# Performance work log

Measured on AMD Instinct MI355X. Metric: run time of the kernel, lower is better.

## Reference

```python
import jax, jax.numpy as jnp
import numpy as np

B, N, C = 4, 4096, 256
H, D, K = 8, 32, 16  # heads, dim_head, knn


def setup_inputs() -> dict:
    key = jax.random.key(0)
    ks = jax.random.split(key, 7)
    s = 1.0 / np.sqrt(C)
    return {
        "x": jax.random.normal(ks[0], (B, N, C), dtype=jnp.float32),
        "Wq": jax.random.normal(ks[1], (C, H * D), dtype=jnp.float32) * s,
        "bq": jnp.zeros((H * D,), dtype=jnp.float32),
        "Wk": jax.random.normal(ks[2], (C, H * D), dtype=jnp.float32) * s,
        "bk": jnp.zeros((H * D,), dtype=jnp.float32),
        "Wv": jax.random.normal(ks[3], (C, H * D), dtype=jnp.float32) * s,
        "bv": jnp.zeros((H * D,), dtype=jnp.float32),
    }


def _knn_indices(x):
    # squared euclidean distances per batch: [B, N, N]
    sq = jnp.sum(x * x, axis=-1)
    d2 = sq[:, :, None] + sq[:, None, :] - 2.0 * jnp.einsum("bnc,bmc->bnm", x, x)
    # exclude self-loops (loop=False)
    eye = jnp.eye(x.shape[1], dtype=bool)
    d2 = jnp.where(eye[None], jnp.inf, d2)
    # k nearest neighbors (smallest distance)
    _, idx = jax.lax.top_k(-d2, K)  # [B, N, K]
    return idx


def reference(x, Wq, bq, Wk, bk, Wv, bv):
    idx = _knn_indices(x)  # [B, N, K] neighbor (source) node ids per target node
    # gather neighbor features: [B, N, K, C]
    xj = jax.vmap(lambda xb, ib: xb[ib])(x, idx)
    q = (x @ Wq + bq).reshape(B, N, H, D)           # target-node queries
    ke = (xj @ Wk + bk).reshape(B, N, K, H, D)      # per-edge keys
    ve = (xj @ Wv + bv).reshape(B, N, K, H, D)      # per-edge values
    scale = 1.0 / np.sqrt(D)
    scores = jnp.einsum("bnhd,bnkhd->bnkh", q, ke) * scale
    alpha = jax.nn.softmax(scores, axis=2)          # softmax over each node's K neighbors
    out = jnp.einsum("bnkh,bnkhd->bnhd", alpha, ve)
    return out.reshape(B, N, H * D)
```

## Files before the change

kernel.cpp:

```cpp
#include <hip/hip_runtime.h>
#include <cstdint>
#include <cstddef>

#define N_ 4096
#define C_ 256

typedef _Float16 h8 __attribute__((ext_vector_type(8)));
typedef _Float16 h4 __attribute__((ext_vector_type(4)));
typedef float f4 __attribute__((ext_vector_type(4)));

__device__ __forceinline__ void gl2lds16(const void* g, void* l) {
  __builtin_amdgcn_global_load_lds((const __attribute__((address_space(1))) void*)g,
                                   (__attribute__((address_space(3))) void*)l, 16, 0, 0);
}

__device__ __forceinline__ void ce_asc(double& a, double& b) {
  double mn = fmin(a, b), mx = fmax(a, b);
  a = mn; b = mx;
}

__device__ __forceinline__ void sort8_asc(double* c) {
#pragma unroll
  for (int k = 2; k <= 8; k <<= 1)
#pragma unroll
    for (int j = k >> 1; j > 0; j >>= 1)
#pragma unroll
      for (int i = 0; i < 8; i++) {
        int l = i ^ j;
        if (l > i) {
          bool up = ((i & k) == 0);
          double a = c[i], b = c[l];
          double mn = fmin(a, b), mx = fmax(a, b);
          c[i] = up ? mn : mx;
          c[l] = up ? mx : mn;
        }
      }
}

__device__ __forceinline__ void merge8_top16(double* karr, const double* c) {
#pragma unroll
  for (int i = 0; i < 8; i++)
    karr[8 + i] = fmin(karr[8 + i], c[7 - i]);
#pragma unroll
  for (int j = 8; j > 0; j >>= 1)
#pragma unroll
    for (int i = 0; i < 16; i++) {
      int l = i ^ j;
      if (l > i) ce_asc(karr[i], karr[l]);
    }
}

__device__ __forceinline__ void merge16d(double* a, const double* b) {
#pragma unroll
  for (int i = 0; i < 16; i++) a[i] = fmin(a[i], b[15 - i]);
#pragma unroll
  for (int j = 8; j > 0; j >>= 1)
#pragma unroll
    for (int i = 0; i < 16; i++) {
      int l = i ^ j;
      if (l > i) {
        double mn = fmin(a[i], a[l]), mx = fmax(a[i], a[l]);
        a[i] = mn; a[l] = mx;
      }
    }
}

__global__ __launch_bounds__(256) void k_prep(const float* __restrict__ x,
                                              float* __restrict__ sq,
                                              _Float16* __restrict__ xh,
                                              _Float16* __restrict__ xl) {
  int wave = threadIdx.x >> 6, lane = threadIdx.x & 63;
  int row = blockIdx.x * 4 + wave;
  size_t off = (size_t)row * C_ + lane * 4;
  float4 v = *(const float4*)(x + off);
  h4 hi; hi[0] = (_Float16)v.x; hi[1] = (_Float16)v.y;
         hi[2] = (_Float16)v.z; hi[3] = (_Float16)v.w;
  h4 lo; lo[0] = (_Float16)(v.x - (float)hi[0]); lo[1] = (_Float16)(v.y - (float)hi[1]);
         lo[2] = (_Float16)(v.z - (float)hi[2]); lo[3] = (_Float16)(v.w - (float)hi[3]);
  *(h4*)(xh + off) = hi;
  *(h4*)(xl + off) = lo;
  float s = v.x * v.x + v.y * v.y + v.z * v.z + v.w * v.w;
  s += __shfl_xor(s, 32); s += __shfl_xor(s, 16); s += __shfl_xor(s, 8);
  s += __shfl_xor(s, 4);  s += __shfl_xor(s, 2);  s += __shfl_xor(s, 1);
  if (lane == 0) sq[row] = s;
}

__global__ __launch_bounds__(256) void k_wsplit(const float* __restrict__ Wq,
                                                const float* __restrict__ Wk,
                                                const float* __restrict__ Wv,
                                                _Float16* __restrict__ wh,
                                                _Float16* __restrict__ wl) {
  int g = blockIdx.x * 256 + threadIdx.x;
  int m = g >> 16, e = g & 65535;
  int k = e >> 8, j = e & 255;
  const float* W = (m == 0) ? Wq : ((m == 1) ? Wk : Wv);
  float v = W[k * 256 + j];
  _Float16 hi = (_Float16)v;
  _Float16 lo = (_Float16)(v - (float)hi);
  wh[m * 65536 + j * 256 + k] = hi;
  wl[m * 65536 + j * 256 + k] = lo;
}

__global__ __launch_bounds__(256, 3) void k_proj(const _Float16* __restrict__ xh,
                                                 const _Float16* __restrict__ xl,
                                                 const _Float16* __restrict__ wh,
                                                 const _Float16* __restrict__ wl,
                                                 const float* __restrict__ bqp,
                                                 const float* __restrict__ bkp,
                                                 const float* __restrict__ bvp,
                                                 float* __restrict__ qf,
                                                 float* __restrict__ kf,
                                                 float* __restrict__ vf) {
  int tid = threadIdx.x;
  int bid = blockIdx.x;
  int m   = bid >> 8;
  int rb  = (bid >> 1) & 127;
  int cp  = bid & 1;
  int wave = tid >> 6, lane = tid & 63, quad = lane >> 4, l16 = lane & 15;
  const float* bb = (m == 0) ? bqp : ((m == 1) ? bkp : bvp);
  float* dst      = (m == 0) ? qf  : ((m == 1) ? kf  : vf);
  int row0 = rb * 128 + wave * 32;

  h8 Ah[2][8], Al[2][8];
#pragma unroll
  for (int rt = 0; rt < 2; rt++)
#pragma unroll
    for (int kc = 0; kc < 8; kc++) {
      size_t off = (size_t)(row0 + rt * 16 + l16) * C_ + kc * 32 + quad * 8;
      Ah[rt][kc] = *(const h8*)(xh + off);
      Al[rt][kc] = *(const h8*)(xl + off);
    }
  const _Float16* whm = wh + (size_t)m * 65536;
  const _Float16* wlm = wl + (size_t)m * 65536;

  f4 acc[2][8];
#pragma unroll
  for (int rt = 0; rt < 2; rt++)
#pragma unroll
    for (int ct = 0; ct < 8; ct++) acc[rt][ct] = f4{0.f, 0.f, 0.f, 0.f};
#pragma unroll
  for (int kc = 0; kc < 8; kc++) {
#pragma unroll
    for (int ct = 0; ct < 8; ct++) {
      int col = cp * 128 + ct * 16 + l16;
      h8 bh = *(const h8*)(whm + (size_t)col * 256 + kc * 32 + quad * 8);
      h8 bl = *(const h8*)(wlm + (size_t)col * 256 + kc * 32 + quad * 8);
#pragma unroll
      for (int rt = 0; rt < 2; rt++) {
        acc[rt][ct] = __builtin_amdgcn_mfma_f32_16x16x32_f16(Ah[rt][kc], bh, acc[rt][ct], 0, 0, 0);
        acc[rt][ct] = __builtin_amdgcn_mfma_f32_16x16x32_f16(Ah[rt][kc], bl, acc[rt][ct], 0, 0, 0);
        acc[rt][ct] = __builtin_amdgcn_mfma_f32_16x16x32_f16(Al[rt][kc], bh, acc[rt][ct], 0, 0, 0);
      }
    }
  }
#pragma unroll
  for (int rt = 0; rt < 2; rt++)
#pragma unroll
    for (int ct = 0; ct < 8; ct++) {
      int col = cp * 128 + ct * 16 + l16;
      float bias = bb[col];
#pragma unroll
      for (int i = 0; i < 4; i++) {
        int r = row0 + rt * 16 + quad * 4 + i;
        dst[(size_t)r * C_ + col] = acc[rt][ct][i] + bias;
      }
    }
}

__global__ __launch_bounds__(256, 2) void k_knn(const _Float16* __restrict__ xh,
                                                const _Float16* __restrict__ xl,
                                                const float* __restrict__ sq,
                                                double* __restrict__ pd) {
  __shared__ __align__(16) _Float16 Bh[2][16 * 528];
  __shared__ __align__(16) _Float16 Bl[2][16 * 528];
  __shared__ __align__(16) float sc[4][16 * 36];

  int tid = threadIdx.x;
  int wave = tid >> 6, lane = tid & 63, quad = lane >> 4, l16 = lane & 15;
  int bid = blockIdx.x;
  int s4 = bid & 3, tile = (bid >> 2) & 31, b = bid >> 7;
  int bN = b * N_, n0 = tile * 128, src0g = s4 * 1024;

  h8 Ah[2][8], Al[2][8];
  int tb = bN + n0 + wave * 32;
#pragma unroll
  for (int rt = 0; rt < 2; rt++)
#pragma unroll
    for (int kc = 0; kc < 8; kc++) {
      size_t off = (size_t)(tb + rt * 16 + l16) * C_ + kc * 32 + quad * 8;
      Ah[rt][kc] = *(const h8*)(xh + off);
      Al[rt][kc] = *(const h8*)(xl + off);
    }
  float sqT[2][4];
#pragma unroll
  for (int rt = 0; rt < 2; rt++)
#pragma unroll
    for (int i = 0; i < 4; i++)
      sqT[rt][i] = sq[tb + rt * 16 + quad * 4 + i];

  double karr[16];
#pragma unroll
  for (int p = 0; p < 16; p++) karr[p] = 1e300;
  int rloc = lane & 31;
  int half = lane >> 5;
  int rown = wave * 32 + rloc;
  int rt_owner = rloc >> 4;
  int rl = rloc & 15;

  {
    const _Float16* gh = xh + (size_t)(bN + src0g) * C_ + lane * 8;
    const _Float16* gl = xl + (size_t)(bN + src0g) * C_ + lane * 8;
#pragma unroll
    for (int k = 0; k < 4; k++) {
      int seg = wave * 4 + k;
      gl2lds16(gh + seg * 512, &Bh[0][seg * 528]);
      gl2lds16(gl + seg * 512, &Bl[0][seg * 528]);
    }
  }

  int hb0 = ((l16 >> 1) * 528) + ((l16 & 1) * 256) + quad * 8;
  int hb1 = (((16 + l16) >> 1) * 528) + ((l16 & 1) * 256) + quad * 8;

#pragma unroll 1
  for (int ch = 0; ch < 32; ch++) {
    int src0 = src0g + ch * 32;
    int buf = ch & 1;
    __syncthreads();

    if (ch < 31) {
      int srcn = src0 + 32;
      const _Float16* gh = xh + (size_t)(bN + srcn) * C_ + lane * 8;
      const _Float16* gl = xl + (size_t)(bN + srcn) * C_ + lane * 8;
#pragma unroll
      for (int k = 0; k < 4; k++) {
        int seg = wave * 4 + k;
        gl2lds16(gh + seg * 512, &Bh[buf ^ 1][seg * 528]);
        gl2lds16(gl + seg * 512, &Bl[buf ^ 1][seg * 528]);
      }
    }
    float sqc0 = sq[bN + src0 + l16];
    float sqc1 = sq[bN + src0 + 16 + l16];

    f4 acc[2][2];
#pragma unroll
    for (int rt = 0; rt < 2; rt++)
#pragma unroll
      for (int ct = 0; ct < 2; ct++) acc[rt][ct] = f4{0.f, 0.f, 0.f, 0.f};
#pragma unroll
    for (int kc = 0; kc < 8; kc++) {
      h8 bh0 = *(const h8*)(&Bh[buf][hb0 + kc * 32]);
      h8 bh1 = *(const h8*)(&Bh[buf][hb1 + kc * 32]);
      h8 bl0 = *(const h8*)(&Bl[buf][hb0 + kc * 32]);
      h8 bl1 = *(const h8*)(&Bl[buf][hb1 + kc * 32]);
#pragma unroll
      for (int rt = 0; rt < 2; rt++) {
        acc[rt][0] = __builtin_amdgcn_mfma_f32_16x16x32_f16(Ah[rt][kc], bh0, acc[rt][0], 0, 0, 0);
        acc[rt][0] = __builtin_amdgcn_mfma_f32_16x16x32_f16(Ah[rt][kc], bl0, acc[rt][0], 0, 0, 0);
        acc[rt][0] = __builtin_amdgcn_mfma_f32_16x16x32_f16(Al[rt][kc], bh0, acc[rt][0], 0, 0, 0);
        acc[rt][1] = __builtin_amdgcn_mfma_f32_16x16x32_f16(Ah[rt][kc], bh1, acc[rt][1], 0, 0, 0);
        acc[rt][1] = __builtin_amdgcn_mfma_f32_16x16x32_f16(Ah[rt][kc], bl1, acc[rt][1], 0, 0, 0);
        acc[rt][1] = __builtin_amdgcn_mfma_f32_16x16x32_f16(Al[rt][kc], bh1, acc[rt][1], 0, 0, 0);
      }
    }

    float dv[16];
#pragma unroll
    for (int rt = 0; rt < 2; rt++) {
#pragma unroll
      for (int ct = 0; ct < 2; ct++) {
        int c = ct * 16 + l16;
        float sqSr = ct ? sqc1 : sqc0;
#pragma unroll
        for (int i = 0; i < 4; i++) {
          int r = wave * 32 + rt * 16 + quad * 4 + i;
          float d2 = sqT[rt][i] + sqSr - 2.0f * acc[rt][ct][i];
          if (n0 + r == src0 + c) d2 = 1e38f;
          sc[wave][(quad * 4 + i) * 36 + c] = d2;
        }
      }
      if (rt_owner == rt) {
#pragma unroll
        for (int j = 0; j < 4; j++)
          *(float4*)&dv[j * 4] = *(const float4*)(&sc[wave][rl * 36 + half * 16 + j * 4]);
      }
      asm volatile("" ::: "memory");
    }

#pragma unroll
    for (int bt = 0; bt < 2; bt++) {
      double c8[8];
#pragma unroll
      for (int j = 0; j < 8; j++) {
        double key = (double)dv[bt * 8 + j];
        c8[j] = __longlong_as_double(__double_as_longlong(key) |
                                     (unsigned)(src0 + half * 16 + bt * 8 + j));
      }
      sort8_asc(c8);
      merge8_top16(karr, c8);
    }
  }

  __syncthreads();
  double* scd = (double*)&Bh[0][0];
  if (half) {
#pragma unroll
    for (int p = 0; p < 16; p++) scd[rown * 17 + p] = karr[p];
  }
  __syncthreads();
  if (!half) {
#pragma unroll
    for (int i = 0; i < 16; i++)
      karr[i] = fmin(karr[i], scd[rown * 17 + (15 - i)]);
#pragma unroll
    for (int j = 8; j > 0; j >>= 1)
#pragma unroll
      for (int i = 0; i < 16; i++) {
        int l = i ^ j;
        if (l > i) ce_asc(karr[i], karr[l]);
      }
#pragma unroll
    for (int p = 0; p < 16; p++)
      pd[((size_t)bid * 128 + rown) * 16 + p] = karr[p];
  }
}

__global__ __launch_bounds__(64) void k_kmerge(const double* __restrict__ pd,
                                               int* __restrict__ idxo) {
  int g = blockIdx.x * 64 + threadIdx.x;
  int b = g >> 12, n = g & 4095;
  int tile = n >> 7, r = n & 127;
  size_t base = (size_t)(((b * 32 + tile) * 4) * 128 + r) * 16;

  double acc[16], other[16];
#pragma unroll
  for (int p = 0; p < 16; p++) acc[p] = pd[base + p];
#pragma unroll
  for (int s = 1; s < 4; s++) {
    size_t bs = base + (size_t)s * 128 * 16;
#pragma unroll
    for (int p = 0; p < 16; p++) other[p] = pd[bs + p];
    merge16d(acc, other);
  }
#pragma unroll
  for (int k = 0; k < 16; k++)
    idxo[(size_t)g * 16 + k] = (int)(__double_as_longlong(acc[k]) & 0xFFF);
}

__global__ __launch_bounds__(256) void k_attn(const float* __restrict__ qf,
                                              const float* __restrict__ kf,
                                              const float* __restrict__ vf,
                                              const int* __restrict__ idxv,
                                              float* __restrict__ out) {
  int wave = threadIdx.x >> 6, lane = threadIdx.x & 63;
  int g = blockIdx.x * 4 + wave;
  int bN = (g >> 12) << 12;
  float4 q4 = *(const float4*)(qf + (size_t)g * C_ + lane * 4);
  int my = idxv[(size_t)g * 16 + (lane & 15)];
  const float scale = 0.17677669529663687f;

  float s[16];
  float4 vv[16];
#pragma unroll
  for (int j = 0; j < 16; j++) {
    int nb = __shfl(my, j);
    size_t base = (size_t)(bN + nb) * C_ + lane * 4;
    float4 k4 = *(const float4*)(kf + base);
    vv[j] = *(const float4*)(vf + base);
    float p = k4.x * q4.x + k4.y * q4.y + k4.z * q4.z + k4.w * q4.w;
    p += __shfl_xor(p, 1); p += __shfl_xor(p, 2); p += __shfl_xor(p, 4);
    s[j] = p * scale;
  }
  float mx = s[0];
#pragma unroll
  for (int j = 1; j < 16; j++) mx = fmaxf(mx, s[j]);
  float den = 0.f;
#pragma unroll
  for (int j = 0; j < 16; j++) { s[j] = __expf(s[j] - mx); den += s[j]; }
  float inv = 1.0f / den;
  float4 o; o.x = 0.f; o.y = 0.f; o.z = 0.f; o.w = 0.f;
#pragma unroll
  for (int j = 0; j < 16; j++) {
    float w = s[j] * inv;
    o.x = fmaf(w, vv[j].x, o.x); o.y = fmaf(w, vv[j].y, o.y);
    o.z = fmaf(w, vv[j].z, o.z); o.w = fmaf(w, vv[j].w, o.w);
  }
  *(float4*)(out + (size_t)g * C_ + lane * 4) = o;
}

extern "C" void kernel_launch(void* const* d_in, const int* in_sizes, int n_in,
                              void* d_out, int out_size, void* d_ws, size_t ws_size,
                              hipStream_t stream) {
  const float* x  = (const float*)d_in[0];
  const float* Wq = (const float*)d_in[1];
  const float* bq = (const float*)d_in[2];
  const float* Wk = (const float*)d_in[3];
  const float* bk = (const float*)d_in[4];
  const float* Wv = (const float*)d_in[5];
  const float* bv = (const float*)d_in[6];
  float* out = (float*)d_out;

  char* ws = (char*)d_ws;
  float*     sqp  = (float*)(ws + 0);
  _Float16*  xh   = (_Float16*)(ws + 65536);
  _Float16*  xl   = (_Float16*)(ws + 8454144);
  float*     qf   = (float*)(ws + 16842752);
  float*     kf   = (float*)(ws + 33619968);
  float*     vf   = (float*)(ws + 50397184);
  double*    pd   = (double*)(ws + 67174400);
  int*       idxb = (int*)  (ws + 75563008);
  _Float16*  whf  = (_Float16*)(ws + 76611584);
  _Float16*  wlf  = (_Float16*)(ws + 77004800);

  k_prep  <<<4096, 256, 0, stream>>>(x, sqp, xh, xl);
  k_wsplit<<<768,  256, 0, stream>>>(Wq, Wk, Wv, whf, wlf);
  k_proj  <<<768,  256, 0, stream>>>(xh, xl, whf, wlf, bq, bk, bv, qf, kf, vf);
  k_knn   <<<512,  256, 0, stream>>>(xh, xl, sqp, pd);
  k_kmerge<<<256,  64,  0, stream>>>(pd, idxb);
  k_attn  <<<4096, 256, 0, stream>>>(qf, kf, vf, idxb, out);
}
```

Measured before the change: 291.8 us.

## Transpose kNN MFMA so each lane owns a target, dropping LDS score shuffle

Reorganizes k_knn into 8 waves of 16 targets each. The MFMA operands are swapped so each lane's accumulator holds distances for its own target column. This removes the per-chunk LDS scratch round-trip that previously moved scores to the thread owning each row, and source squared norms now arrive through LDS via async global-to-LDS loads. Each lane sorts 8 candidates per chunk instead of 16, and the per-target top-16 lists held by four lanes are combined with a two-step LDS merge tree. The cost is more threads per block, extra barriers at the end, and higher register pressure under launch_bounds(512,4).

```diff
diff --git a/kernel.cpp b/kernel.cpp
--- a/kernel.cpp
+++ b/kernel.cpp
@@ -12,6 +12,10 @@
 __device__ __forceinline__ void gl2lds16(const void* g, void* l) {
   __builtin_amdgcn_global_load_lds((const __attribute__((address_space(1))) void*)g,
                                    (__attribute__((address_space(3))) void*)l, 16, 0, 0);
+}
+__device__ __forceinline__ void gl2lds4(const void* g, void* l) {
+  __builtin_amdgcn_global_load_lds((const __attribute__((address_space(1))) void*)g,
+                                   (__attribute__((address_space(3))) void*)l, 4, 0, 0);
 }
 
 __device__ __forceinline__ void ce_asc(double& a, double& b) {
@@ -167,13 +171,13 @@
     }
 }
 
-__global__ __launch_bounds__(256, 2) void k_knn(const _Float16* __restrict__ xh,
+__global__ __launch_bounds__(512, 4) void k_knn(const _Float16* __restrict__ xh,
                                                 const _Float16* __restrict__ xl,
                                                 const float* __restrict__ sq,
                                                 double* __restrict__ pd) {
   __shared__ __align__(16) _Float16 Bh[2][16 * 528];
   __shared__ __align__(16) _Float16 Bl[2][16 * 528];
-  __shared__ __align__(16) float sc[4][16 * 36];
+  __shared__ __align__(16) float sqLds[2][64];
 
   int tid = threadIdx.x;
   int wave = tid >> 6, lane = tid & 63, quad = lane >> 4, l16 = lane & 15;
@@ -181,45 +185,35 @@
   int s4 = bid & 3, tile = (bid >> 2) & 31, b = bid >> 7;
   int bN = b * N_, n0 = tile * 128, src0g = s4 * 1024;
 
-  h8 Ah[2][8], Al[2][8];
-  int tb = bN + n0 + wave * 32;
-#pragma unroll
-  for (int rt = 0; rt < 2; rt++)
-#pragma unroll
-    for (int kc = 0; kc < 8; kc++) {
-      size_t off = (size_t)(tb + rt * 16 + l16) * C_ + kc * 32 + quad * 8;
-      Ah[rt][kc] = *(const h8*)(xh + off);
-      Al[rt][kc] = *(const h8*)(xl + off);
-    }
-  float sqT[2][4];
-#pragma unroll
-  for (int rt = 0; rt < 2; rt++)
-#pragma unroll
-    for (int i = 0; i < 4; i++)
-      sqT[rt][i] = sq[tb + rt * 16 + quad * 4 + i];
+  h8 Th[8], Tl[8];
+  int tgt_loc = n0 + wave * 16 + l16;
+  int tgtg = bN + tgt_loc;
+#pragma unroll
+  for (int kc = 0; kc < 8; kc++) {
+    size_t off = (size_t)tgtg * C_ + kc * 32 + quad * 8;
+    Th[kc] = *(const h8*)(xh + off);
+    Tl[kc] = *(const h8*)(xl + off);
+  }
+  float sqT = sq[tgtg];
 
   double karr[16];
 #pragma unroll
   for (int p = 0; p < 16; p++) karr[p] = 1e300;
-  int rloc = lane & 31;
-  int half = lane >> 5;
-  int rown = wave * 32 + rloc;
-  int rt_owner = rloc >> 4;
-  int rl = rloc & 15;
 
   {
     const _Float16* gh = xh + (size_t)(bN + src0g) * C_ + lane * 8;
     const _Float16* gl = xl + (size_t)(bN + src0g) * C_ + lane * 8;
 #pragma unroll
-    for (int k = 0; k < 4; k++) {
-      int seg = wave * 4 + k;
+    for (int k = 0; k < 2; k++) {
+      int seg = wave * 2 + k;
       gl2lds16(gh + seg * 512, &Bh[0][seg * 528]);
       gl2lds16(gl + seg * 512, &Bl[0][seg * 528]);
     }
-  }
-
-  int hb0 = ((l16 >> 1) * 528) + ((l16 & 1) * 256) + quad * 8;
-  int hb1 = (((16 + l16) >> 1) * 528) + ((l16 & 1) * 256) + quad * 8;
+    if (wave == 0) gl2lds4(sq + bN + src0g + (lane & 31), &sqLds[0][0]);
+  }
+
+  int base0 = (l16 >> 1) * 528 + (l16 & 1) * 256 + quad * 8;
+  int base1 = base0 + 8 * 528;
 
 #pragma unroll 1
   for (int ch = 0; ch < 32; ch++) {
@@ -232,95 +226,79 @@
       const _Float16* gh = xh + (size_t)(bN + srcn) * C_ + lane * 8;
       const _Float16* gl = xl + (size_t)(bN + srcn) * C_ + lane * 8;
 #pragma unroll
-      for (int k = 0; k < 4; k++) {
-        int seg = wave * 4 + k;
+      for (int k = 0; k < 2; k++) {
+        int seg = wave * 2 + k;
         gl2lds16(gh + seg * 512, &Bh[buf ^ 1][seg * 528]);
         gl2lds16(gl + seg * 512, &Bl[buf ^ 1][seg * 528]);
       }
-    }
-    float sqc0 = sq[bN + src0 + l16];
-    float sqc1 = sq[bN + src0 + 16 + l16];
-
-    f4 acc[2][2];
-#pragma unroll
-    for (int rt = 0; rt < 2; rt++)
-#pragma unroll
-      for (int ct = 0; ct < 2; ct++) acc[rt][ct] = f4{0.f, 0.f, 0.f, 0.f};
+      if (wave == 0) gl2lds4(sq + bN + srcn + (lane & 31), &sqLds[buf ^ 1][0]);
+    }
+
+    f4 acc[2];
+    acc[0] = f4{0.f, 0.f, 0.f, 0.f};
+    acc[1] = f4{0.f, 0.f, 0.f, 0.f};
 #pragma unroll
     for (int kc = 0; kc < 8; kc++) {
-      h8 bh0 = *(const h8*)(&Bh[buf][hb0 + kc * 32]);
-      h8 bh1 = *(const h8*)(&Bh[buf][hb1 + kc * 32]);
-      h8 bl0 = *(const h8*)(&Bl[buf][hb0 + kc * 32]);
-      h8 bl1 = *(const h8*)(&Bl[buf][hb1 + kc * 32]);
-#pragma unroll
-      for (int rt = 0; rt < 2; rt++) {
-        acc[rt][0] = __builtin_amdgcn_mfma_f32_16x16x32_f16(Ah[rt][kc], bh0, acc[rt][0], 0, 0, 0);
-        acc[rt][0] = __builtin_amdgcn_mfma_f32_16x16x32_f16(Ah[rt][kc], bl0, acc[rt][0], 0, 0, 0);
-        acc[rt][0] = __builtin_amdgcn_mfma_f32_16x16x32_f16(Al[rt][kc], bh0, acc[rt][0], 0, 0, 0);
-        acc[rt][1] = __builtin_amdgcn_mfma_f32_16x16x32_f16(Ah[rt][kc], bh1, acc[rt][1], 0, 0, 0);
-        acc[rt][1] = __builtin_amdgcn_mfma_f32_16x16x32_f16(Ah[rt][kc], bl1, acc[rt][1], 0, 0, 0);
-        acc[rt][1] = __builtin_amdgcn_mfma_f32_16x16x32_f16(Al[rt][kc], bh1, acc[rt][1], 0, 0, 0);
-      }
-    }
-
-    float dv[16];
-#pragma unroll
-    for (int rt = 0; rt < 2; rt++) {
-#pragma unroll
-      for (int ct = 0; ct < 2; ct++) {
-        int c = ct * 16 + l16;
-        float sqSr = ct ? sqc1 : sqc0;
-#pragma unroll
-        for (int i = 0; i < 4; i++) {
-          int r = wave * 32 + rt * 16 + quad * 4 + i;
-          float d2 = sqT[rt][i] + sqSr - 2.0f * acc[rt][ct][i];
-          if (n0 + r == src0 + c) d2 = 1e38f;
-          sc[wave][(quad * 4 + i) * 36 + c] = d2;
-        }
-      }
-      if (rt_owner == rt) {
-#pragma unroll
-        for (int j = 0; j < 4; j++)
-          *(float4*)&dv[j * 4] = *(const float4*)(&sc[wave][rl * 36 + half * 16 + j * 4]);
-      }
-      asm volatile("" ::: "memory");
-    }
-
-#pragma unroll
-    for (int bt = 0; bt < 2; bt++) {
-      double c8[8];
-#pragma unroll
-      for (int j = 0; j < 8; j++) {
-        double key = (double)dv[bt * 8 + j];
-        c8[j] = __longlong_as_double(__double_as_longlong(key) |
-                                     (unsigned)(src0 + half * 16 + bt * 8 + j));
-      }
-      sort8_asc(c8);
-      merge8_top16(karr, c8);
-    }
+      h8 sh0 = *(const h8*)(&Bh[buf][base0 + kc * 32]);
+      h8 sh1 = *(const h8*)(&Bh[buf][base1 + kc * 32]);
+      h8 sl0 = *(const h8*)(&Bl[buf][base0 + kc * 32]);
+      h8 sl1 = *(const h8*)(&Bl[buf][base1 + kc * 32]);
+      acc[0] = __builtin_amdgcn_mfma_f32_16x16x32_f16(sh0, Th[kc], acc[0], 0, 0, 0);
+      acc[1] = __builtin_amdgcn_mfma_f32_16x16x32_f16(sh1, Th[kc], acc[1], 0, 0, 0);
+      acc[0] = __builtin_amdgcn_mfma_f32_16x16x32_f16(sh0, Tl[kc], acc[0], 0, 0, 0);
+      acc[1] = __builtin_amdgcn_mfma_f32_16x16x32_f16(sh1, Tl[kc], acc[1], 0, 0, 0);
+      acc[0] = __builtin_amdgcn_mfma_f32_16x16x32_f16(sl0, Th[kc], acc[0], 0, 0, 0);
+      acc[1] = __builtin_amdgcn_mfma_f32_16x16x32_f16(sl1, Th[kc], acc[1], 0, 0, 0);
+    }
+
+    const float* sqB = (const float*)&sqLds[buf][0];
+    double c8[8];
+#pragma unroll
+    for (int st = 0; st < 2; st++)
+#pragma unroll
+      for (int i = 0; i < 4; i++) {
+        int sidx = st * 16 + quad * 4 + i;
+        float d2 = sqT + sqB[sidx] - 2.0f * acc[st][i];
+        if (tgt_loc == src0 + sidx) d2 = 1e38f;
+        double key = (double)d2;
+        c8[st * 4 + i] = __longlong_as_double(__double_as_longlong(key) |
+                                              (unsigned)(src0 + sidx));
+      }
+    sort8_asc(c8);
+    merge8_top16(karr, c8);
   }
 
   __syncthreads();
-  double* scd = (double*)&Bh[0][0];
-  if (half) {
-#pragma unroll
-    for (int p = 0; p < 16; p++) scd[rown * 17 + p] = karr[p];
+  double* ex = (double*)&Bh[0][0];
+  if (quad >= 2) {
+    int slot = wave * 32 + (quad - 2) * 16 + l16;
+#pragma unroll
+    for (int p = 0; p < 16; p++) ex[slot * 16 + p] = karr[p];
   }
   __syncthreads();
-  if (!half) {
-#pragma unroll
-    for (int i = 0; i < 16; i++)
-      karr[i] = fmin(karr[i], scd[rown * 17 + (15 - i)]);
-#pragma unroll
-    for (int j = 8; j > 0; j >>= 1)
-#pragma unroll
-      for (int i = 0; i < 16; i++) {
-        int l = i ^ j;
-        if (l > i) ce_asc(karr[i], karr[l]);
-      }
+  if (quad < 2) {
+    double other[16];
+    int slot = wave * 32 + quad * 16 + l16;
+#pragma unroll
+    for (int p = 0; p < 16; p++) other[p] = ex[slot * 16 + p];
+    merge16d(karr, other);
+  }
+  __syncthreads();
+  if (quad == 1) {
+    int slot = wave * 16 + l16;
+#pragma unroll
+    for (int p = 0; p < 16; p++) ex[slot * 16 + p] = karr[p];
+  }
+  __syncthreads();
+  if (quad == 0) {
+    double other[16];
+    int slot = wave * 16 + l16;
+#pragma unroll
+    for (int p = 0; p < 16; p++) other[p] = ex[slot * 16 + p];
+    merge16d(karr, other);
 #pragma unroll
     for (int p = 0; p < 16; p++)
-      pd[((size_t)bid * 128 + rown) * 16 + p] = karr[p];
+      pd[((size_t)bid * 128 + wave * 16 + l16) * 16 + p] = karr[p];
   }
 }
 
@@ -414,7 +392,7 @@
   k_prep  <<<4096, 256, 0, stream>>>(x, sqp, xh, xl);
   k_wsplit<<<768,  256, 0, stream>>>(Wq, Wk, Wv, whf, wlf);
   k_proj  <<<768,  256, 0, stream>>>(xh, xl, whf, wlf, bq, bk, bv, qf, kf, vf);
-  k_knn   <<<512,  256, 0, stream>>>(xh, xl, sqp, pd);
+  k_knn   <<<512,  512, 0, stream>>>(xh, xl, sqp, pd);
   k_kmerge<<<256,  64,  0, stream>>>(pd, idxb);
   k_attn  <<<4096, 256, 0, stream>>>(qf, kf, vf, idxb, out);
 }
```

Measured after the change: 397.9 us. +36.3%, slower.
